# Kernel tuning notes

Hardware: AMD Instinct MI355X
Metric: run time of the kernel (lower is better)

The kernel has to match this reference:

```python
import jax, jax.numpy as jnp
import numpy as np

NUM_BINS = 256
WS = 5          # ssim_window_size
SIGMA = 1.5
LEVELS = 5
MS_WEIGHTS = jnp.asarray(np.array([0.0448, 0.2856, 0.3001, 0.2363, 0.1333], dtype=np.float32))


def _gauss_window():
    x = np.arange(WS) - WS // 2
    g = np.exp(-(x.astype(np.float64) ** 2) / (2.0 * SIGMA ** 2))
    g = g / g.sum()
    return jnp.asarray(np.outer(g, g), dtype=jnp.float32)  # (WS, WS)


def _conv_same(x, w):
    # x: (H, W), w: (WS, WS); 'SAME' pad == torch padding=WS//2 for odd WS
    return jax.lax.conv_general_dilated(x[None, None], w[None, None], (1, 1), 'SAME')[0, 0]


def _rgb_to_lab(img):
    # img: (3, H, W) in [0,1] -> normalized LAB (3, H, W)  (CURL ImageProcessing.rgb_to_lab)
    H, W = img.shape[1], img.shape[2]
    x = jnp.transpose(img, (2, 1, 0)).reshape(-1, 3)  # (W*H, 3)
    lin = jnp.where(x <= 0.04045, x / 12.92,
                    ((jnp.maximum(x, 1e-4) + 0.055) / 1.055) ** 2.4)
    rgb2xyz = jnp.array([[0.412453, 0.212671, 0.019334],
                         [0.357580, 0.715160, 0.119193],
                         [0.180423, 0.072169, 0.950227]], dtype=img.dtype)
    xyz = lin @ rgb2xyz
    xyz = xyz * jnp.array([1.0 / 0.950456, 1.0, 1.0 / 1.088754], dtype=img.dtype)
    eps = 6.0 / 29.0
    f = jnp.where(xyz <= eps ** 3,
                  xyz / (3.0 * eps ** 2) + 4.0 / 29.0,
                  jnp.maximum(xyz, 1e-4) ** (1.0 / 3.0))
    f2lab = jnp.array([[0.0, 500.0, 0.0],
                       [116.0, -500.0, 200.0],
                       [0.0, 0.0, -200.0]], dtype=img.dtype)
    lab = f @ f2lab + jnp.array([-16.0, 0.0, 0.0], dtype=img.dtype)
    lab = jnp.transpose(lab.reshape(W, H, 3), (2, 1, 0))  # (3, H, W)
    return jnp.stack([lab[0] / 100.0,
                      (lab[1] / 110.0 + 1.0) / 2.0,
                      (lab[2] / 110.0 + 1.0) / 2.0])


def _histogram(img):
    # img: (3, H, W) in [0,1] -> per-channel 256-bin count histogram (3, NUM_BINS)
    idx = jnp.clip(jnp.floor(img * NUM_BINS).astype(jnp.int32), 0, NUM_BINS - 1)
    per_ch = lambda ix: jnp.zeros((NUM_BINS,), jnp.float32).at[ix.reshape(-1)].add(1.0)
    return jax.vmap(per_ch)(idx)


def _ssim(i1, i2, w):
    # i1, i2: (H, W) single-channel images
    mu1 = _conv_same(i1, w)
    mu2 = _conv_same(i2, w)
    s1 = _conv_same(i1 * i1, w) - mu1 * mu1
    s2 = _conv_same(i2 * i2, w) - mu2 * mu2
    s12 = _conv_same(i1 * i2, w) - mu1 * mu2
    C1, C2 = 0.01 ** 2, 0.03 ** 2
    ssim_map = ((2.0 * mu1 * mu2 + C1) * (2.0 * s12 + C2)) / \
               ((mu1 * mu1 + mu2 * mu2 + C1) * (s1 + s2 + C2))
    cs = jnp.mean((2.0 * s12 + C2) / (s1 + s2 + C2))
    return ssim_map.mean(), cs


def _avg_pool2(x):
    H, W = x.shape
    return x.reshape(H // 2, 2, W // 2, 2).mean(axis=(1, 3))


def _msssim(i1, i2, w):
    mssim, mcs = [], []
    for _ in range(LEVELS):
        s, cs = _ssim(i1, i2, w)
        mssim.append(s)
        mcs.append(cs)
        i1 = _avg_pool2(i1)
        i2 = _avg_pool2(i2)
    mssim = (jnp.stack(mssim) + 1.0) / 2.0
    mcs = (jnp.stack(mcs) + 1.0) / 2.0
    return jnp.prod(mcs[:LEVELS - 1] ** MS_WEIGHTS[:LEVELS - 1]) * mssim[LEVELS - 1] ** MS_WEIGHTS[LEVELS - 1]


def _forward(input_image_batch, predicted_img_batch, target_img_batch):
    pred_lab = jnp.clip(jax.vmap(_rgb_to_lab)(predicted_img_batch), 0.0, 1.0)
    tgt_lab = jnp.clip(jax.vmap(_rgb_to_lab)(target_img_batch), 0.0, 1.0)

    # histogram loss: original loop does h_i = (h_{i-1} + l1_i + 1) / 2; closed form below
    hp = jax.vmap(_histogram)(pred_lab)   # (B, 3, NUM_BINS)
    ht = jax.vmap(_histogram)(tgt_lab)
    l1_hist = jnp.mean(jnp.abs(hp - ht), axis=(1, 2))  # (B,)
    n = l1_hist.shape[0]
    wgt = 2.0 ** (jnp.arange(n, dtype=jnp.float32) - n)  # 2^{-(n-i)}
    hist_loss = jnp.sum(wgt * (l1_hist + 1.0))

    # MS-SSIM on L channel, per image (is_identity=True -> no variational_prediction)
    window = _gauss_window()
    ms = jax.vmap(lambda a, b: _msssim(a, b, window))(pred_lab[:, 0], tgt_lab[:, 0])
    ssim_loss = jnp.mean(1.0 - ms)

    lab_l1 = jnp.mean(jnp.abs(pred_lab - tgt_lab))  # mean of per-image means (same-size imgs)

    H, W = input_image_batch.shape[2], input_image_batch.shape[3]
    scaler = H * W / 20.0
    hist_loss = hist_loss / n / scaler
    lab_loss = lab_l1 + hist_loss
    return lab_loss.reshape(1, 1), ssim_loss.reshape(1, 1)


def setup_inputs():
    key = jax.random.key(0)
    k1, k2, k3 = jax.random.split(key, 3)
    B, C, H, W = 8, 3, 512, 512
    return {
        'input_image_batch': jax.random.uniform(k1, (B, C, H, W), jnp.float32),
        'predicted_img_batch': jax.random.uniform(k2, (B, C, H, W), jnp.float32),
        'target_img_batch': jax.random.uniform(k3, (B, C, H, W), jnp.float32),
        'is_identity': 1,
    }


def reference(input_image_batch, predicted_img_batch, target_img_batch, is_identity):
    return _forward(input_image_batch, predicted_img_batch, target_img_batch)
```

## Files before the change

### kernel.cpp

```cpp
#include <hip/hip_runtime.h>
#include <math.h>

#define B 8
#define IMH 512
#define IMW 512
#define HW (IMH*IMW)
#define NBINS 256

#define PYR_PER_IMG (65536 + 16384 + 4096 + 1024)
#define PYR_OFF_L1 0
#define PYR_OFF_L2 65536
#define PYR_OFF_L3 81920
#define PYR_OFF_L4 86016

#define OFF_PPYR 0
#define OFF_TPYR (B*PYR_PER_IMG)
#define OFF_HISTPART (2*B*PYR_PER_IMG)
#define OFF_LABPART  (OFF_HISTPART + B*256*768)
#define OFF_ACC      (OFF_LABPART + 2048)

typedef float f2 __attribute__((ext_vector_type(2)));

__device__ __forceinline__ f2 mkf2(float a, float b) { f2 r; r.x = a; r.y = b; return r; }
__device__ __forceinline__ f2 shfl_down_f2(f2 v, int d) {
    return mkf2(__shfl_down(v.x, d, 64), __shfl_down(v.y, d, 64));
}
__device__ __forceinline__ f2 shfl_f2(f2 v, int src) {
    return mkf2(__shfl(v.x, src, 64), __shfl(v.y, src, 64));
}
__device__ __forceinline__ f2 clamp01_f2(f2 a) {
    a.x = fminf(fmaxf(a.x, 0.0f), 1.0f);
    a.y = fminf(fmaxf(a.y, 0.0f), 1.0f);
    return a;
}

__device__ __forceinline__ float fastpow(float x, float y) {
    return __builtin_amdgcn_exp2f(y * __builtin_amdgcn_logf(x));
}

__device__ __forceinline__ void rgb2lab_pk(f2 r, f2 g, f2 b, f2 lab[3]) {
    f2 v[3] = {r, g, b};
    f2 lin[3];
    #pragma unroll
    for (int c = 0; c < 3; ++c) {
        f2 x = v[c];
        float hx = fastpow((fmaxf(x.x, 1e-4f) + 0.055f) * (float)(1.0/1.055), 2.4f);
        float hy = fastpow((fmaxf(x.y, 1e-4f) + 0.055f) * (float)(1.0/1.055), 2.4f);
        lin[c].x = (x.x <= 0.04045f) ? x.x * (float)(1.0/12.92) : hx;
        lin[c].y = (x.y <= 0.04045f) ? x.y * (float)(1.0/12.92) : hy;
    }
    f2 X = 0.412453f*lin[0] + 0.357580f*lin[1] + 0.180423f*lin[2];
    f2 Y = 0.212671f*lin[0] + 0.715160f*lin[1] + 0.072169f*lin[2];
    f2 Z = 0.019334f*lin[0] + 0.119193f*lin[1] + 0.950227f*lin[2];
    X = X * (float)(1.0/0.950456);
    Z = Z * (float)(1.0/1.088754);
    const float eps3   = (float)((6.0/29.0)*(6.0/29.0)*(6.0/29.0));
    const float rd3e2  = (float)(1.0/(3.0*(6.0/29.0)*(6.0/29.0)));
    const float c429   = (float)(4.0/29.0);
    f2 xyz[3] = {X, Y, Z};
    f2 f[3];
    #pragma unroll
    for (int c = 0; c < 3; ++c) {
        float ax = xyz[c].x, ay = xyz[c].y;
        f[c].x = (ax <= eps3) ? (ax * rd3e2 + c429) : fastpow(fmaxf(ax, 1e-4f), (float)(1.0/3.0));
        f[c].y = (ay <= eps3) ? (ay * rd3e2 + c429) : fastpow(fmaxf(ay, 1e-4f), (float)(1.0/3.0));
    }
    f2 L  = 116.0f*f[1] - 16.0f;
    f2 A  = 500.0f*f[0] - 500.0f*f[1];
    f2 Bc = 200.0f*f[1] - 200.0f*f[2];
    lab[0] = L * 0.01f;
    lab[1] = (A * (float)(1.0/110.0) + 1.0f) * 0.5f;
    lab[2] = (Bc * (float)(1.0/110.0) + 1.0f) * 0.5f;
}

#define TST 37

__device__ __forceinline__ void conv_ssim(const f2* tile, int t, float& ssum, float& csum) {
    double gd[5]; double gs = 0.0;
    #pragma unroll
    for (int i = 0; i < 5; ++i) { gd[i] = exp(-(double)((i-2)*(i-2)) / 4.5); gs += gd[i]; }
    float gw[5];
    #pragma unroll
    for (int i = 0; i < 5; ++i) gw[i] = (float)(gd[i] / gs);

    int lx = t & 31;
    int yg = t >> 5;

    f2 rA[8], rB[8];
    float r12[8];
    #pragma unroll
    for (int k = 0; k < 8; ++k) {
        int row = yg * 4 + k;
        const f2* p = &tile[row * TST + lx];
        f2 sA = {0.f, 0.f}, sB = {0.f, 0.f};
        float s12 = 0.f;
        #pragma unroll
        for (int dx = 0; dx < 5; ++dx) {
            f2 av = p[dx];
            float wv = gw[dx];
            sA += wv * av;
            f2 sq = av * av;
            sB += wv * sq;
            s12 = fmaf(wv, av.x * av.y, s12);
        }
        rA[k] = sA; rB[k] = sB; r12[k] = s12;
    }

    const float C1 = (float)(0.01 * 0.01);
    const float C2 = (float)(0.03 * 0.03);
    ssum = 0.f; csum = 0.f;
    #pragma unroll
    for (int j = 0; j < 4; ++j) {
        f2 mA = {0.f, 0.f}, mB = {0.f, 0.f};
        float m12 = 0.f;
        #pragma unroll
        for (int k = 0; k < 5; ++k) {
            float wv = gw[k];
            mA += wv * rA[j + k];
            mB += wv * rB[j + k];
            m12 = fmaf(wv, r12[j + k], m12);
        }
        float m1 = mA.x, m2 = mA.y;
        float v1  = mB.x - m1 * m1;
        float v2  = mB.y - m2 * m2;
        float v12 = m12 - m1 * m2;
        float n12 = 2.0f * v12 + C2;
        float rd2 = __builtin_amdgcn_rcpf(v1 + v2 + C2);
        float rd1 = __builtin_amdgcn_rcpf(m1*m1 + m2*m2 + C1);
        csum = fmaf(n12, rd2, csum);
        ssum += (2.0f*m1*m2 + C1) * n12 * rd1 * rd2;
    }
}

__device__ __forceinline__ void halo_coords(int h, int& hr, int& hc) {
    if (h < 72)       { hr = h / 36;            hc = h % 36; }
    else if (h < 144) { int u = h - 72;  hr = 34 + u / 36; hc = u % 36; }
    else              { int u = h - 144; hr = 2 + (u >> 2); int q = u & 3; hc = (q < 2) ? q : 32 + q; }
}

__global__ void lab_ssim0_kernel(const float* __restrict__ pred,
                                 const float* __restrict__ tgt,
                                 unsigned* __restrict__ histPart,
                                 float* __restrict__ labPart,
                                 double* __restrict__ accs,
                                 float* __restrict__ ppyr,
                                 float* __restrict__ tpyr) {
    __shared__ f2 ls[36 * TST];
    __shared__ unsigned lhist[6 * NBINS];
    __shared__ f2 s1[16 * 16];
    __shared__ float red12[12];

    int t  = threadIdx.x;
    int b  = blockIdx.y;
    int bx = blockIdx.x;

    for (int i = t; i < 6 * NBINS; i += 256) lhist[i] = 0;
    __syncthreads();

    int tile = ((bx & 7) << 5) | (bx >> 3);
    int tx0 = (tile & 15) << 5;
    int ty0 = (tile >> 4) << 5;
    int r   = t >> 3;
    int c4  = (t & 7) << 2;
    int gy  = ty0 + r;

    const float* pimg = pred + (size_t)b * 3 * HW;
    const float* timg = tgt  + (size_t)b * 3 * HW;
    size_t ibase = (size_t)gy * IMW + tx0 + c4;

    float prA[4], pgA[4], pbA[4], trA[4], tgA[4], tbA[4];
    *(float4*)&prA[0] = *(const float4*)(pimg + ibase);
    *(float4*)&pgA[0] = *(const float4*)(pimg + ibase + HW);
    *(float4*)&pbA[0] = *(const float4*)(pimg + ibase + 2*HW);
    *(float4*)&trA[0] = *(const float4*)(timg + ibase);
    *(float4*)&tgA[0] = *(const float4*)(timg + ibase + HW);
    *(float4*)&tbA[0] = *(const float4*)(timg + ibase + 2*HW);

    int hr0, hc0;
    halo_coords(t, hr0, hc0);
    int hy0 = ty0 - 2 + hr0;
    int hx0 = tx0 - 2 + hc0;
    bool hv0 = ((unsigned)hy0 < 512u) && ((unsigned)hx0 < 512u);
    size_t ho = hv0 ? ((size_t)hy0 * IMW + hx0) : 0;
    float h_pr = pimg[ho], h_pg = pimg[ho + HW], h_pb = pimg[ho + 2*HW];
    float h_tr = timg[ho], h_tg = timg[ho + HW], h_tb = timg[ho + 2*HW];

    float l1 = 0.0f;
    f2 pL[4];
    #pragma unroll
    for (int k = 0; k < 4; ++k) {
        f2 lab[3];
        rgb2lab_pk(mkf2(prA[k], trA[k]), mkf2(pgA[k], tgA[k]), mkf2(pbA[k], tbA[k]), lab);
        #pragma unroll
        for (int c = 0; c < 3; ++c) {
            f2 lc = clamp01_f2(lab[c]);
            l1 += fabsf(lc.x - lc.y);
            int ip = min(max((int)floorf(lc.x * (float)NBINS), 0), NBINS - 1);
            int it = min(max((int)floorf(lc.y * (float)NBINS), 0), NBINS - 1);
            atomicAdd(&lhist[c * NBINS + ip], 1u);
            atomicAdd(&lhist[(3 + c) * NBINS + it], 1u);
            if (c == 0) pL[k] = lc;
        }
        ls[(r + 2) * TST + (c4 + 2 + k)] = pL[k];
    }

    {
        f2 lab[3];
        rgb2lab_pk(mkf2(h_pr, h_tr), mkf2(h_pg, h_tg), mkf2(h_pb, h_tb), lab);
        f2 Lv = hv0 ? clamp01_f2(lab[0]) : mkf2(0.f, 0.f);
        ls[hr0 * TST + hc0] = Lv;
    }
    if (t < 16) {
        int hr, hc;
        halo_coords(256 + t, hr, hc);
        int hy = ty0 - 2 + hr;
        int hx = tx0 - 2 + hc;
        f2 Lv = {0.f, 0.f};
        if ((unsigned)hy < 512u && (unsigned)hx < 512u) {
            size_t o = (size_t)hy * IMW + hx;
            f2 lab[3];
            rgb2lab_pk(mkf2(pimg[o], timg[o]),
                       mkf2(pimg[o + HW], timg[o + HW]),
                       mkf2(pimg[o + 2*HW], timg[o + 2*HW]), lab);
            Lv = clamp01_f2(lab[0]);
        }
        ls[hr * TST + hc] = Lv;
    }
    __syncthreads();

    unsigned* hp = histPart + ((size_t)b * 256 + bx) * 768;
    for (int i = t; i < 768; i += 256)
        hp[i] = (lhist[2*i] & 0xFFFFu) | (lhist[2*i + 1] << 16);

    float* pyrP = ppyr + (size_t)b * PYR_PER_IMG;
    float* pyrT = tpyr + (size_t)b * PYR_PER_IMG;
    f2 ph0 = pL[0] + pL[1], ph1 = pL[2] + pL[3];
    f2 ph0b = shfl_down_f2(ph0, 8);
    f2 ph1b = shfl_down_f2(ph1, 8);
    if ((t & 8) == 0) {
        int y1 = r >> 1;
        int x1 = (t & 7) << 1;
        f2 v0 = 0.25f * (ph0 + ph0b);
        f2 v1 = 0.25f * (ph1 + ph1b);
        s1[y1 * 16 + x1]     = v0;
        s1[y1 * 16 + x1 + 1] = v1;
        int g1 = ((ty0 >> 1) + y1) * 256 + (tx0 >> 1) + x1;
        *(float2*)&pyrP[PYR_OFF_L1 + g1] = make_float2(v0.x, v1.x);
        *(float2*)&pyrT[PYR_OFF_L1 + g1] = make_float2(v0.y, v1.y);
    }
    __syncthreads();

    float ssum, csum;
    conv_ssim(ls, t, ssum, csum);

    if (t < 64) {
        int y2 = t >> 3, x2 = t & 7;
        const f2* s = &s1[(2*y2) * 16 + 2*x2];
        f2 v2 = 0.25f * (s[0] + s[1] + s[16] + s[17]);
        pyrP[PYR_OFF_L2 + ((ty0 >> 2) + y2) * 128 + (tx0 >> 2) + x2] = v2.x;
        pyrT[PYR_OFF_L2 + ((ty0 >> 2) + y2) * 128 + (tx0 >> 2) + x2] = v2.y;

        int y3 = (t >> 2) & 3, x3 = t & 3;
        f2 v3 = 0.25f * (shfl_f2(v2, (2*y3)*8 + 2*x3)     + shfl_f2(v2, (2*y3)*8 + 2*x3 + 1) +
                         shfl_f2(v2, (2*y3+1)*8 + 2*x3)   + shfl_f2(v2, (2*y3+1)*8 + 2*x3 + 1));
        if (t < 16) {
            pyrP[PYR_OFF_L3 + ((ty0 >> 3) + y3) * 64 + (tx0 >> 3) + x3] = v3.x;
            pyrT[PYR_OFF_L3 + ((ty0 >> 3) + y3) * 64 + (tx0 >> 3) + x3] = v3.y;
        }
        int y4 = (t >> 1) & 1, x4 = t & 1;
        f2 v4 = 0.25f * (shfl_f2(v3, (2*y4)*4 + 2*x4)     + shfl_f2(v3, (2*y4)*4 + 2*x4 + 1) +
                         shfl_f2(v3, (2*y4+1)*4 + 2*x4)   + shfl_f2(v3, (2*y4+1)*4 + 2*x4 + 1));
        if (t < 4) {
            pyrP[PYR_OFF_L4 + ((ty0 >> 4) + y4) * 32 + (tx0 >> 4) + x4] = v4.x;
            pyrT[PYR_OFF_L4 + ((ty0 >> 4) + y4) * 32 + (tx0 >> 4) + x4] = v4.y;
        }
    }

    int lane = t & 63;
    int wid  = t >> 6;
    #pragma unroll
    for (int o = 32; o >= 1; o >>= 1) {
        l1   += __shfl_down(l1, o, 64);
        ssum += __shfl_down(ssum, o, 64);
        csum += __shfl_down(csum, o, 64);
    }
    if (lane == 0) {
        red12[wid * 3 + 0] = l1;
        red12[wid * 3 + 1] = ssum;
        red12[wid * 3 + 2] = csum;
    }
    __syncthreads();
    if (t < 4) {
        float a0 = red12[t * 3 + 0];
        float a1 = red12[t * 3 + 1];
        float a2 = red12[t * 3 + 2];
        #pragma unroll
        for (int o = 2; o >= 1; o >>= 1) {
            a0 += __shfl_down(a0, o, 64);
            a1 += __shfl_down(a1, o, 64);
            a2 += __shfl_down(a2, o, 64);
        }
        if (t == 0) {
            labPart[b * 256 + bx] = a0;
            atomicAdd(&accs[b * 5 + 0], (double)a1);
            atomicAdd(&accs[40 + b * 5 + 0], (double)a2);
        }
    }
}

__global__ void tail_kernel(const float* __restrict__ ppyr,
                            const float* __restrict__ tpyr,
                            const unsigned* __restrict__ histPart,
                            const float* __restrict__ labPart,
                            double* __restrict__ accs,
                            float* __restrict__ out) {
    __shared__ f2 tls[36 * TST];
    __shared__ float red12[12];
    __shared__ int dLo[256];
    __shared__ int dHi[256];
    int t = threadIdx.x;
    int bx = blockIdx.x;
    double* histL1acc = accs + 80;
    double* labSumD   = accs + 88;
    unsigned* counter = (unsigned*)(accs + 89);

    if (bx < 48) {
        int b  = bx / 6;
        int w  = (bx % 6) * 64 + (t & 63);
        int ck = t >> 6;
        const unsigned* p = histPart + (size_t)b * 256 * 768 + (size_t)(ck * 64) * 768;
        unsigned sPlo = 0, sPhi = 0, sTlo = 0, sThi = 0;
        #pragma unroll 8
        for (int i = 0; i < 64; ++i) {
            unsigned wP = p[(size_t)i * 768 + w];
            unsigned wT = p[(size_t)i * 768 + 384 + w];
            sPlo += wP & 0xFFFFu;  sPhi += wP >> 16;
            sTlo += wT & 0xFFFFu;  sThi += wT >> 16;
        }
        dLo[t] = (int)sPlo - (int)sTlo;
        dHi[t] = (int)sPhi - (int)sThi;
        __syncthreads();
        if (t < 64) {
            int lo = dLo[t] + dLo[t + 64] + dLo[t + 128] + dLo[t + 192];
            int hi = dHi[t] + dHi[t + 64] + dHi[t + 128] + dHi[t + 192];
            float val = fabsf((float)lo) + fabsf((float)hi);
            #pragma unroll
            for (int o = 32; o >= 1; o >>= 1) val += __shfl_down(val, o, 64);
            if (t == 0) atomicAdd(&histL1acc[b], (double)val);
        }
        __syncthreads();
    } else if (bx == 48) {
        float s = 0.0f;
        #pragma unroll
        for (int k = 0; k < 8; ++k) s += labPart[t + k * 256];
        int lane = t & 63;
        int wid  = t >> 6;
        #pragma unroll
        for (int o = 32; o >= 1; o >>= 1) s += __shfl_down(s, o, 64);
        if (lane == 0) red12[wid * 3] = s;
        __syncthreads();
        if (t == 0) labSumD[0] = (double)(red12[0] + red12[3] + red12[6] + red12[9]);
    } else {
        int cb = bx - 49;
        int b = cb / 85;
        int sub = cb - b * 85;
        int lvl, pblk;
        if (sub < 64)      { lvl = 1; pblk = sub; }
        else if (sub < 80) { lvl = 2; pblk = sub - 64; }
        else if (sub < 84) { lvl = 3; pblk = sub - 80; }
        else               { lvl = 4; pblk = 0; }

        const int offs[5] = {0, PYR_OFF_L1, PYR_OFF_L2, PYR_OFF_L3, PYR_OFF_L4};
        int w = 512 >> lvl;
        const float* i1 = ppyr + (size_t)b * PYR_PER_IMG + offs[lvl];
        const float* i2 = tpyr + (size_t)b * PYR_PER_IMG + offs[lvl];

        int tprShift = 4 - lvl;
        int ty0 = (pblk >> tprShift) << 5;
        int tx0 = (pblk & ((1 << tprShift) - 1)) << 5;

        for (int i = t; i < 36 * 36; i += 256) {
            int r = i / 36, c = i % 36;
            int gy = ty0 - 2 + r;
            int gx = tx0 - 2 + c;
            bool ok = ((unsigned)gy < (unsigned)w) && ((unsigned)gx < (unsigned)w);
            int gi = gy * w + gx;
            tls[r * TST + c] = ok ? mkf2(i1[gi], i2[gi]) : mkf2(0.f, 0.f);
        }
        __syncthreads();

        float ssum, csum;
        conv_ssim(tls, t, ssum, csum);

        int lane = t & 63;
        int wid  = t >> 6;
        #pragma unroll
        for (int o = 32; o >= 1; o >>= 1) {
            ssum += __shfl_down(ssum, o, 64);
            csum += __shfl_down(csum, o, 64);
        }
        if (lane == 0) {
            red12[wid * 3 + 0] = ssum;
            red12[wid * 3 + 1] = csum;
        }
        __syncthreads();
        if (t < 4) {
            float a1 = red12[t * 3 + 0];
            float a2 = red12[t * 3 + 1];
            #pragma unroll
            for (int o = 2; o >= 1; o >>= 1) {
                a1 += __shfl_down(a1, o, 64);
                a2 += __shfl_down(a2, o, 64);
            }
            if (t == 0) {
                atomicAdd(&accs[b * 5 + lvl], (double)a1);
                atomicAdd(&accs[40 + b * 5 + lvl], (double)a2);
            }
        }
    }

    __syncthreads();
    if (t < 64) {
        unsigned old = 0;
        if (t == 0) { __threadfence(); old = atomicAdd(counter, 1u); }
        old = __shfl(old, 0, 64);
        if (old == 728u) {
            __threadfence();
            volatile double* vacc = accs;
            const float msw[5] = {0.0448f, 0.2856f, 0.3001f, 0.2363f, 0.1333f};
            const float npix[5] = {(float)HW, (float)(HW/4), (float)(HW/16),
                                   (float)(HW/64), (float)(HW/256)};
            float histc = 0.0f, lossc = 0.0f;
            if (t < 8) {
                int b = t;
                float l1 = (float)(vacc[80 + b] / (double)(3 * NBINS));
                float wgt = __builtin_amdgcn_exp2f((float)(b - B));
                histc = wgt * (l1 + 1.0f);
                float ms = 1.0f;
                #pragma unroll
                for (int l = 0; l < 4; ++l) {
                    float cs = (float)(vacc[40 + b * 5 + l] / (double)npix[l]);
                    ms *= fastpow((cs + 1.0f) * 0.5f, msw[l]);
                }
                float sm = (float)(vacc[b * 5 + 4] / (double)npix[4]);
                ms *= fastpow((sm + 1.0f) * 0.5f, msw[4]);
                lossc = 1.0f - ms;
            }
            #pragma unroll
            for (int o = 4; o >= 1; o >>= 1) {
                histc += __shfl_down(histc, o, 64);
                lossc += __shfl_down(lossc, o, 64);
            }
            if (t == 0) {
                float scaler = (float)HW / 20.0f;
                float hist_loss = histc / (float)B / scaler;
                float lab_l1 = (float)(vacc[88] / (double)((size_t)B * 3 * HW));
                out[0] = lab_l1 + hist_loss;
                out[1] = lossc / (float)B;
            }
        }
    }
}

extern "C" void kernel_launch(void* const* d_in, const int* in_sizes, int n_in,
                              void* d_out, int out_size, void* d_ws, size_t ws_size,
                              hipStream_t stream) {
    const float* pred = (const float*)d_in[1];
    const float* tgt  = (const float*)d_in[2];
    float* ws_f = (float*)d_ws;

    float* ppyr  = ws_f + OFF_PPYR;
    float* tpyr  = ws_f + OFF_TPYR;
    unsigned* histPart = (unsigned*)(ws_f + OFF_HISTPART);
    float* labPart = ws_f + OFF_LABPART;
    double* accs = (double*)(ws_f + OFF_ACC);
    float* out = (float*)d_out;

    hipMemsetAsync(accs, 0, 90 * sizeof(double), stream);

    lab_ssim0_kernel<<<dim3(256, B), 256, 0, stream>>>(pred, tgt, histPart, labPart,
                                                       accs, ppyr, tpyr);

    tail_kernel<<<729, 256, 0, stream>>>(ppyr, tpyr, histPart, labPart, accs, out);
}
```

Before: 138.7 us.

## Replace double atomics and memset with per-block partials and a final reduction kernel

Per-block SSIM/CS sums are now written to per-block partial arrays instead of double-precision atomicAdds, and a small third kernel reduces them and computes the final losses. This removes the memset launch, the atomic counter, and the last-block detection. Level-0 SSIM skips computing the luminance term, which was unused since only the CS value matters at that level. The cost is an extra kernel launch.

```diff
diff --git a/kernel.cpp b/kernel.cpp
--- a/kernel.cpp
+++ b/kernel.cpp
@@ -17,7 +17,10 @@
 #define OFF_TPYR (B*PYR_PER_IMG)
 #define OFF_HISTPART (2*B*PYR_PER_IMG)
 #define OFF_LABPART  (OFF_HISTPART + B*256*768)
-#define OFF_ACC      (OFF_LABPART + 2048)
+#define OFF_CSP      (OFF_LABPART + B*256)
+#define OFF_LVLS     (OFF_CSP + B*256)
+#define OFF_LVLC     (OFF_LVLS + B*85)
+#define OFF_HISTL1   (OFF_LVLC + B*85)
 
 typedef float f2 __attribute__((ext_vector_type(2)));
 
@@ -75,6 +78,7 @@
 
 #define TST 37
 
+template<bool WANT_S>
 __device__ __forceinline__ void conv_ssim(const f2* tile, int t, float& ssum, float& csum) {
     double gd[5]; double gs = 0.0;
     #pragma unroll
@@ -108,7 +112,8 @@
 
     const float C1 = (float)(0.01 * 0.01);
     const float C2 = (float)(0.03 * 0.03);
-    ssum = 0.f; csum = 0.f;
+    if constexpr (WANT_S) ssum = 0.f;
+    csum = 0.f;
     #pragma unroll
     for (int j = 0; j < 4; ++j) {
         f2 mA = {0.f, 0.f}, mB = {0.f, 0.f};
@@ -126,9 +131,11 @@
         float v12 = m12 - m1 * m2;
         float n12 = 2.0f * v12 + C2;
         float rd2 = __builtin_amdgcn_rcpf(v1 + v2 + C2);
-        float rd1 = __builtin_amdgcn_rcpf(m1*m1 + m2*m2 + C1);
         csum = fmaf(n12, rd2, csum);
-        ssum += (2.0f*m1*m2 + C1) * n12 * rd1 * rd2;
+        if constexpr (WANT_S) {
+            float rd1 = __builtin_amdgcn_rcpf(m1*m1 + m2*m2 + C1);
+            ssum += (2.0f*m1*m2 + C1) * n12 * rd1 * rd2;
+        }
     }
 }
 
@@ -142,7 +149,7 @@
                                  const float* __restrict__ tgt,
                                  unsigned* __restrict__ histPart,
                                  float* __restrict__ labPart,
-                                 double* __restrict__ accs,
+                                 float* __restrict__ csPart,
                                  float* __restrict__ ppyr,
                                  float* __restrict__ tpyr) {
     __shared__ f2 ls[36 * TST];
@@ -250,8 +257,8 @@
     }
     __syncthreads();
 
-    float ssum, csum;
-    conv_ssim(ls, t, ssum, csum);
+    float sdummy, csum;
+    conv_ssim<false>(ls, t, sdummy, csum);
 
     if (t < 64) {
         int y2 = t >> 3, x2 = t & 7;
@@ -281,29 +288,24 @@
     #pragma unroll
     for (int o = 32; o >= 1; o >>= 1) {
         l1   += __shfl_down(l1, o, 64);
-        ssum += __shfl_down(ssum, o, 64);
         csum += __shfl_down(csum, o, 64);
     }
     if (lane == 0) {
-        red12[wid * 3 + 0] = l1;
-        red12[wid * 3 + 1] = ssum;
-        red12[wid * 3 + 2] = csum;
+        red12[wid * 2 + 0] = l1;
+        red12[wid * 2 + 1] = csum;
     }
     __syncthreads();
     if (t < 4) {
-        float a0 = red12[t * 3 + 0];
-        float a1 = red12[t * 3 + 1];
-        float a2 = red12[t * 3 + 2];
+        float a0 = red12[t * 2 + 0];
+        float a2 = red12[t * 2 + 1];
         #pragma unroll
         for (int o = 2; o >= 1; o >>= 1) {
             a0 += __shfl_down(a0, o, 64);
-            a1 += __shfl_down(a1, o, 64);
             a2 += __shfl_down(a2, o, 64);
         }
         if (t == 0) {
             labPart[b * 256 + bx] = a0;
-            atomicAdd(&accs[b * 5 + 0], (double)a1);
-            atomicAdd(&accs[40 + b * 5 + 0], (double)a2);
+            csPart[b * 256 + bx]  = a2;
         }
     }
 }
@@ -311,18 +313,15 @@
 __global__ void tail_kernel(const float* __restrict__ ppyr,
                             const float* __restrict__ tpyr,
                             const unsigned* __restrict__ histPart,
-                            const float* __restrict__ labPart,
-                            double* __restrict__ accs,
-                            float* __restrict__ out) {
+                            float* __restrict__ lvlS,
+                            float* __restrict__ lvlC,
+                            float* __restrict__ histL1p) {
     __shared__ f2 tls[36 * TST];
     __shared__ float red12[12];
     __shared__ int dLo[256];
     __shared__ int dHi[256];
     int t = threadIdx.x;
     int bx = blockIdx.x;
-    double* histL1acc = accs + 80;
-    double* labSumD   = accs + 88;
-    unsigned* counter = (unsigned*)(accs + 89);
 
     if (bx < 48) {
         int b  = bx / 6;
@@ -346,22 +345,10 @@
             float val = fabsf((float)lo) + fabsf((float)hi);
             #pragma unroll
             for (int o = 32; o >= 1; o >>= 1) val += __shfl_down(val, o, 64);
-            if (t == 0) atomicAdd(&histL1acc[b], (double)val);
-        }
-        __syncthreads();
-    } else if (bx == 48) {
-        float s = 0.0f;
-        #pragma unroll
-        for (int k = 0; k < 8; ++k) s += labPart[t + k * 256];
-        int lane = t & 63;
-        int wid  = t >> 6;
-        #pragma unroll
-        for (int o = 32; o >= 1; o >>= 1) s += __shfl_down(s, o, 64);
-        if (lane == 0) red12[wid * 3] = s;
-        __syncthreads();
-        if (t == 0) labSumD[0] = (double)(red12[0] + red12[3] + red12[6] + red12[9]);
+            if (t == 0) histL1p[bx] = val;
+        }
     } else {
-        int cb = bx - 49;
+        int cb = bx - 48;
         int b = cb / 85;
         int sub = cb - b * 85;
         int lvl, pblk;
@@ -390,7 +377,7 @@
         __syncthreads();
 
         float ssum, csum;
-        conv_ssim(tls, t, ssum, csum);
+        conv_ssim<true>(tls, t, ssum, csum);
 
         int lane = t & 63;
         int wid  = t >> 6;
@@ -400,64 +387,101 @@
             csum += __shfl_down(csum, o, 64);
         }
         if (lane == 0) {
-            red12[wid * 3 + 0] = ssum;
-            red12[wid * 3 + 1] = csum;
+            red12[wid * 2 + 0] = ssum;
+            red12[wid * 2 + 1] = csum;
         }
         __syncthreads();
         if (t < 4) {
-            float a1 = red12[t * 3 + 0];
-            float a2 = red12[t * 3 + 1];
+            float a1 = red12[t * 2 + 0];
+            float a2 = red12[t * 2 + 1];
             #pragma unroll
             for (int o = 2; o >= 1; o >>= 1) {
                 a1 += __shfl_down(a1, o, 64);
                 a2 += __shfl_down(a2, o, 64);
             }
             if (t == 0) {
-                atomicAdd(&accs[b * 5 + lvl], (double)a1);
-                atomicAdd(&accs[40 + b * 5 + lvl], (double)a2);
+                lvlS[cb] = a1;
+                lvlC[cb] = a2;
             }
         }
     }
-
+}
+
+__global__ void final_kernel(const float* __restrict__ labPart,
+                             const float* __restrict__ csPart,
+                             const float* __restrict__ lvlS,
+                             const float* __restrict__ lvlC,
+                             const float* __restrict__ histL1p,
+                             float* __restrict__ out) {
+    __shared__ double sh[48];
+    __shared__ double wred[4];
+    int t = threadIdx.x;
+
+    {
+        int b = t >> 5, k = t & 31;
+        double s = 0.0;
+        #pragma unroll
+        for (int j = 0; j < 8; ++j) s += (double)csPart[b * 256 + k + 32 * j];
+        #pragma unroll
+        for (int o = 16; o >= 1; o >>= 1) s += __shfl_down(s, o, 32);
+        if (k == 0) sh[b] = s;
+    }
+    {
+        double s = 0.0;
+        #pragma unroll
+        for (int j = 0; j < 8; ++j) s += (double)labPart[t + 256 * j];
+        #pragma unroll
+        for (int o = 32; o >= 1; o >>= 1) s += __shfl_down(s, o, 64);
+        if ((t & 63) == 0) wred[t >> 6] = s;
+    }
+    if (t < 32) {
+        int b = t >> 2, q = t & 3;
+        const int lo[4] = {0, 64, 80, 84};
+        const int hi[4] = {64, 80, 84, 85};
+        const float* src = (q == 3) ? lvlS : lvlC;
+        double s = 0.0;
+        for (int i = lo[q]; i < hi[q]; ++i) s += (double)src[b * 85 + i];
+        sh[8 + q * 8 + b] = s;
+    }
+    if (t < 8) {
+        double s = 0.0;
+        #pragma unroll
+        for (int j = 0; j < 6; ++j) s += (double)histL1p[t * 6 + j];
+        sh[40 + t] = s;
+    }
     __syncthreads();
-    if (t < 64) {
-        unsigned old = 0;
-        if (t == 0) { __threadfence(); old = atomicAdd(counter, 1u); }
-        old = __shfl(old, 0, 64);
-        if (old == 728u) {
-            __threadfence();
-            volatile double* vacc = accs;
-            const float msw[5] = {0.0448f, 0.2856f, 0.3001f, 0.2363f, 0.1333f};
-            const float npix[5] = {(float)HW, (float)(HW/4), (float)(HW/16),
-                                   (float)(HW/64), (float)(HW/256)};
-            float histc = 0.0f, lossc = 0.0f;
-            if (t < 8) {
-                int b = t;
-                float l1 = (float)(vacc[80 + b] / (double)(3 * NBINS));
-                float wgt = __builtin_amdgcn_exp2f((float)(b - B));
-                histc = wgt * (l1 + 1.0f);
-                float ms = 1.0f;
-                #pragma unroll
-                for (int l = 0; l < 4; ++l) {
-                    float cs = (float)(vacc[40 + b * 5 + l] / (double)npix[l]);
-                    ms *= fastpow((cs + 1.0f) * 0.5f, msw[l]);
-                }
-                float sm = (float)(vacc[b * 5 + 4] / (double)npix[4]);
-                ms *= fastpow((sm + 1.0f) * 0.5f, msw[4]);
-                lossc = 1.0f - ms;
-            }
-            #pragma unroll
-            for (int o = 4; o >= 1; o >>= 1) {
-                histc += __shfl_down(histc, o, 64);
-                lossc += __shfl_down(lossc, o, 64);
-            }
-            if (t == 0) {
-                float scaler = (float)HW / 20.0f;
-                float hist_loss = histc / (float)B / scaler;
-                float lab_l1 = (float)(vacc[88] / (double)((size_t)B * 3 * HW));
-                out[0] = lab_l1 + hist_loss;
-                out[1] = lossc / (float)B;
-            }
+
+    if (t < 8) {
+        const float msw[5]  = {0.0448f, 0.2856f, 0.3001f, 0.2363f, 0.1333f};
+        const float npix[5] = {(float)HW, (float)(HW/4), (float)(HW/16),
+                               (float)(HW/64), (float)(HW/256)};
+        int b = t;
+        float l1 = (float)(sh[40 + b] / (double)(3 * NBINS));
+        float wgt = __builtin_amdgcn_exp2f((float)(b - B));
+        float histc = wgt * (l1 + 1.0f);
+        float ms = 1.0f;
+        float cs0 = (float)(sh[b] / (double)npix[0]);
+        ms *= fastpow((cs0 + 1.0f) * 0.5f, msw[0]);
+        #pragma unroll
+        for (int l = 1; l <= 3; ++l) {
+            float cs = (float)(sh[l * 8 + b] / (double)npix[l]);
+            ms *= fastpow((cs + 1.0f) * 0.5f, msw[l]);
+        }
+        float sm = (float)(sh[32 + b] / (double)npix[4]);
+        ms *= fastpow((sm + 1.0f) * 0.5f, msw[4]);
+        float lossc = 1.0f - ms;
+        #pragma unroll
+        for (int o = 4; o >= 1; o >>= 1) {
+            histc += __shfl_down(histc, o, 64);
+            lossc += __shfl_down(lossc, o, 64);
+        }
+        if (t == 0) {
+            double labSum = wred[0] + wred[1] + wred[2] + wred[3];
+            float scaler = (float)HW / 20.0f;
+            float hist_loss = histc / (float)B / scaler;
+            float lab_l1 = (float)(sh[40] * 0.0 + labSum / (double)((size_t)B * 3 * HW));
+            out[0] = lab_l1 + hist_loss;
+            out[1] = lossc / (float)B;
         }
     }
 }
@@ -469,17 +493,21 @@
     const float* tgt  = (const float*)d_in[2];
     float* ws_f = (float*)d_ws;
 
-    float* ppyr  = ws_f + OFF_PPYR;
-    float* tpyr  = ws_f + OFF_TPYR;
+    float* ppyr     = ws_f + OFF_PPYR;
+    float* tpyr     = ws_f + OFF_TPYR;
     unsigned* histPart = (unsigned*)(ws_f + OFF_HISTPART);
-    float* labPart = ws_f + OFF_LABPART;
-    double* accs = (double*)(ws_f + OFF_ACC);
+    float* labPart  = ws_f + OFF_LABPART;
+    float* csPart   = ws_f + OFF_CSP;
+    float* lvlS     = ws_f + OFF_LVLS;
+    float* lvlC     = ws_f + OFF_LVLC;
+    float* histL1p  = ws_f + OFF_HISTL1;
     float* out = (float*)d_out;
 
-    hipMemsetAsync(accs, 0, 90 * sizeof(double), stream);
 
     lab_ssim0_kernel<<<dim3(256, B), 256, 0, stream>>>(pred, tgt, histPart, labPart,
-                                                       accs, ppyr, tpyr);
-
-    tail_kernel<<<729, 256, 0, stream>>>(ppyr, tpyr, histPart, labPart, accs, out);
-}
+                                                       csPart, ppyr, tpyr);
+
+    tail_kernel<<<728, 256, 0, stream>>>(ppyr, tpyr, histPart, lvlS, lvlC, histL1p);
+
+    final_kernel<<<1, 256, 0, stream>>>(labPart, csPart, lvlS, lvlC, histL1p, out);
+}
```

Measured after the change: 129.9 us. 6.4% less time.
